# Optimization experiments

Measured on AMD Instinct MI355X. Metric: run time of the kernel, lower is better.

The kernel has to match this reference:

```python
import jax, jax.numpy as jnp
import numpy as np
import math

N_NODES = 20000
N_EDGES = 320000
DIM = 256
NUM_HEADS = 8


def setup_inputs() -> dict:
    key = jax.random.key(0)
    ks = jax.random.split(key, 8)
    x = jax.random.normal(ks[0], (N_NODES, DIM), dtype=jnp.float32)
    edge_index = jax.random.randint(ks[1], (2, N_EDGES), 0, N_NODES, dtype=jnp.int64)
    edge_attr = jax.random.normal(ks[2], (N_EDGES, DIM), dtype=jnp.float32)
    s = 1.0 / math.sqrt(DIM)
    Wq = jax.random.uniform(ks[3], (DIM, DIM), jnp.float32, -s, s)
    Wk = jax.random.uniform(ks[4], (DIM, DIM), jnp.float32, -s, s)
    Wv = jax.random.uniform(ks[5], (DIM, DIM), jnp.float32, -s, s)
    We = jax.random.uniform(ks[6], (DIM, DIM), jnp.float32, -s, s)
    be = jax.random.uniform(ks[7], (DIM,), jnp.float32, -s, s)
    return {"x": x, "edge_index": edge_index, "edge_attr": edge_attr,
            "Wq": Wq, "Wk": Wk, "Wv": Wv, "We": We, "be": be}


def reference(x, edge_index, edge_attr, Wq, Wk, Wv, We, be):
    N = x.shape[0]
    E = edge_attr.shape[0]
    H = NUM_HEADS
    C = DIM // H  # per-head channels (concat=True)
    src = edge_index[0]  # segment / attention-grouping index
    dst = edge_index[1]
    # Z = edge_attr * x[dst]  -> [E, D]
    Z = edge_attr * x[dst]
    q = x @ Wq.T          # [N, D]
    k = Z @ Wk.T          # [E, D]
    v = Z @ Wv.T          # [E, D]
    edge_out = Z @ We.T + be  # [E, D]
    # split heads
    qh = q.reshape(N, H, C)
    kh = k.reshape(E, H, C)
    vh = v.reshape(E, H, C)
    # per-edge, per-head score: sum(q[src]*k)/sqrt(C)   -> [E, H]
    scores = jnp.einsum('ehc,ehc->eh', qh[src], kh) / math.sqrt(C)
    # segment softmax grouped by src node
    m = jax.ops.segment_max(scores, src, num_segments=N)        # [N, H]
    ex = jnp.exp(scores - m[src])                               # [E, H]
    denom = jax.ops.segment_sum(ex, src, num_segments=N)        # [N, H]
    attn = ex / (denom[src] + 1e-16)                            # [E, H]
    # weighted scatter-sum of values -> [N, H, C] -> [N, D]
    out = jax.ops.segment_sum(attn[:, :, None] * vh, src, num_segments=N)
    out = out.reshape(N, H * C)
    return (out, edge_out)
```

## Files before the change

kernel.cpp:

```cpp
#include <hip/hip_runtime.h>
#include <math.h>

#define NN 20000
#define NE 320000
#define DIM 256

typedef __bf16 bf16x8 __attribute__((ext_vector_type(8)));
typedef float f32x4 __attribute__((ext_vector_type(4)));
typedef int i32x4 __attribute__((ext_vector_type(4)));
typedef unsigned short u16x4 __attribute__((ext_vector_type(4)));

union B8 { i32x4 i; bf16x8 b; };

__device__ __forceinline__ unsigned short f2bf(float f) {
  unsigned int u; __builtin_memcpy(&u, &f, 4);
  u += 0x7fffu + ((u >> 16) & 1u);
  return (unsigned short)(u >> 16);
}
__device__ __forceinline__ float bf2f(unsigned short h) {
  unsigned int u = ((unsigned int)h) << 16;
  float f; __builtin_memcpy(&f, &u, 4);
  return f;
}

#define GLOAD16(gp, lp)                                                        \
  __builtin_amdgcn_global_load_lds(                                            \
      (const __attribute__((address_space(1))) unsigned int*)(gp),             \
      (__attribute__((address_space(3))) unsigned int*)(lp), 16, 0, 0)

__global__ __launch_bounds__(256) void pack_w(const float* __restrict__ W,
                                              unsigned short* __restrict__ wf) {
  int t = blockIdx.x * 256 + threadIdx.x;
  int lane = t & 63, ct = (t >> 6) & 15, ks = t >> 10;
  int col = ct * 16 + (lane & 15);
  int k0 = ks * 32 + (lane >> 4) * 8;
  const float* src = W + col * 256 + k0;
  unsigned int h[8];
#pragma unroll
  for (int j = 0; j < 8; j++) h[j] = f2bf(src[j]);
  i32x4 v;
  v.x = (int)(h[0] | (h[1] << 16));
  v.y = (int)(h[2] | (h[3] << 16));
  v.z = (int)(h[4] | (h[5] << 16));
  v.w = (int)(h[6] | (h[7] << 16));
  ((i32x4*)wf)[t] = v;
}

__global__ __launch_bounds__(256) void zprep(const float* __restrict__ x,
                                             const int* __restrict__ ei,
                                             const float* __restrict__ ea,
                                             unsigned short* __restrict__ zg) {
  int idx = blockIdx.x * 256 + threadIdx.x;
  int e = idx >> 4, c = idx & 15;
  int dst = ei[NE + e];
  const f32x4* ap = (const f32x4*)(ea + (size_t)e * DIM + c * 16);
  const f32x4* xp = (const f32x4*)(x + (size_t)dst * DIM + c * 16);
  unsigned int h[16];
#pragma unroll
  for (int j = 0; j < 4; j++) {
    f32x4 a = ap[j], b = xp[j];
    f32x4 p = a * b;
    h[j * 4 + 0] = f2bf(p.x); h[j * 4 + 1] = f2bf(p.y);
    h[j * 4 + 2] = f2bf(p.z); h[j * 4 + 3] = f2bf(p.w);
  }
  i32x4 o0, o1;
  o0.x = (int)(h[0] | (h[1] << 16));  o0.y = (int)(h[2] | (h[3] << 16));
  o0.z = (int)(h[4] | (h[5] << 16));  o0.w = (int)(h[6] | (h[7] << 16));
  o1.x = (int)(h[8] | (h[9] << 16));  o1.y = (int)(h[10] | (h[11] << 16));
  o1.z = (int)(h[12] | (h[13] << 16)); o1.w = (int)(h[14] | (h[15] << 16));
  i32x4* dp = (i32x4*)(zg + (size_t)e * 512 + c * 16);
  dp[0] = o0; dp[1] = o1;
}

__device__ __forceinline__ void gemm_tile(const unsigned short* zs,
                                          const unsigned short* wf,
                                          int lane, int wv, f32x4 (&acc)[4][4]) {
#pragma unroll 1
  for (int ksI = 0; ksI < 8; ksI++) {
    bf16x8 afr[4], bfr[4];
#pragma unroll
    for (int rt = 0; rt < 4; rt++) {
      int row = rt * 16 + (lane & 15);
      int k = ksI * 32 + (lane >> 4) * 8;
      int byteo = (row * 512 + k * 2) ^ ((row & 7) << 4);
      B8 u; u.i = *(const i32x4*)((const char*)zs + byteo);
      afr[rt] = u.b;
    }
#pragma unroll
    for (int ct = 0; ct < 4; ct++) {
      B8 u; u.i = ((const i32x4*)wf)[ksI * 1024 + (wv * 4 + ct) * 64 + lane];
      bfr[ct] = u.b;
    }
#pragma unroll
    for (int rt = 0; rt < 4; rt++)
#pragma unroll
      for (int ct = 0; ct < 4; ct++)
        acc[rt][ct] = __builtin_amdgcn_mfma_f32_16x16x32_bf16(afr[rt], bfr[ct], acc[rt][ct], 0, 0, 0);
  }
}

__global__ __launch_bounds__(256) void q_kernel(const float* __restrict__ x,
                                                const unsigned short* __restrict__ wf,
                                                float* __restrict__ q) {
  __shared__ unsigned short zs[64 * 256];
  int tid = threadIdx.x, lane = tid & 63, wv = tid >> 6;
  int r0 = blockIdx.x * 64;
  int dcol = lane * 4;
#pragma unroll 4
  for (int rr = 0; rr < 16; rr++) {
    int r = rr * 4 + wv;
    int row = r0 + r;
    f32x4 a = {0.f, 0.f, 0.f, 0.f};
    if (row < NN) a = *(const f32x4*)(x + (size_t)row * DIM + dcol);
    u16x4 z;
    z.x = f2bf(a.x); z.y = f2bf(a.y); z.z = f2bf(a.z); z.w = f2bf(a.w);
    int byteo = (r * 512 + dcol * 2) ^ ((r & 7) << 4);
    *(u16x4*)((char*)zs + byteo) = z;
  }
  __syncthreads();
  f32x4 acc[4][4];
#pragma unroll
  for (int rt = 0; rt < 4; rt++)
#pragma unroll
    for (int ct = 0; ct < 4; ct++) acc[rt][ct] = (f32x4){0.f, 0.f, 0.f, 0.f};
  gemm_tile(zs, wf, lane, wv, acc);
  int cq = lane & 15, rq = lane >> 4;
#pragma unroll
  for (int ct = 0; ct < 4; ct++) {
    int col = wv * 64 + ct * 16 + cq;
#pragma unroll
    for (int rt = 0; rt < 4; rt++) {
#pragma unroll
      for (int j = 0; j < 4; j++) {
        int row = r0 + rt * 16 + rq * 4 + j;
        if (row < NN) q[(size_t)row * DIM + col] = acc[rt][ct][j];
      }
    }
  }
}

__global__ __launch_bounds__(512) void gemm_edge(
    const unsigned short* __restrict__ zg, const int* __restrict__ ei,
    const int* __restrict__ pos,
    const unsigned short* __restrict__ wfk, const unsigned short* __restrict__ wfv,
    const unsigned short* __restrict__ wfe, const float* __restrict__ be,
    const float* __restrict__ q, unsigned short* __restrict__ vws,
    float* __restrict__ sperm, float* __restrict__ edge_out) {
  __shared__ unsigned short zs[128 * 256];
  int tid = threadIdx.x, lane = tid & 63, wv = tid >> 6;
  int wm = wv >> 2, wn = wv & 3;
  int rq = lane >> 4, cl = lane & 15;
  int e0 = blockIdx.x * 128;

  const unsigned short* wfs[3] = {wfv, wfe, wfk};
  i32x4 wbuf[4][4];
  i32x4 zbuf[2][4];
  f32x4 acc[4][4];

#define LOADW(S, SLOT)                                                         \
  {                                                                            \
    const unsigned short* wfp = wfs[(S) >> 3];                                 \
    _Pragma("unroll") for (int a = 0; a < 4; a++)                              \
        wbuf[SLOT][a] =                                                        \
            ((const i32x4*)wfp)[((S) & 7) * 1024 + (wn * 4 + a) * 64 + lane];  \
  }
#define LOADZ(S, SLOT)                                                         \
  {                                                                            \
    _Pragma("unroll") for (int b = 0; b < 4; b++) {                            \
      int row = wm * 64 + b * 16 + cl;                                         \
      int kk = ((S) & 7) * 32 + rq * 8;                                        \
      int byteo = (row * 512 + kk * 2) ^ ((row & 7) << 4);                     \
      zbuf[SLOT][b] = *(const i32x4*)((const char*)zs + byteo);                \
    }                                                                          \
  }
#define GEMM_PASS(P)                                                           \
  _Pragma("unroll") for (int a = 0; a < 4; a++)                                \
      _Pragma("unroll") for (int b = 0; b < 4; b++)                            \
          acc[a][b] = (f32x4){0.f, 0.f, 0.f, 0.f};                             \
  _Pragma("unroll") for (int ks = 0; ks < 8; ks++) {                           \
    const int step = (P) * 8 + ks;                                             \
    if (step + 2 < 24) LOADW(step + 2, (step + 2) & 3);                        \
    if (step + 1 < 24) LOADZ(step + 1, (step + 1) & 1);                        \
    _Pragma("unroll") for (int a = 0; a < 4; a++) {                            \
      B8 w; w.i = wbuf[step & 3][a];                                           \
      _Pragma("unroll") for (int b = 0; b < 4; b++) {                          \
        B8 z; z.i = zbuf[step & 1][b];                                         \
        acc[a][b] = __builtin_amdgcn_mfma_f32_16x16x32_bf16(w.b, z.b,          \
                                                            acc[a][b], 0, 0, 0); \
      }                                                                        \
    }                                                                          \
  }

  {
    int rl = wv * 2 + (lane >> 5);
    int c = lane & 31;
#pragma unroll
    for (int s = 0; s < 8; s++) {
      int r = s * 16 + rl;
      const unsigned short* gp = zg + (size_t)(e0 + r) * 512 + ((c ^ (r & 7)) * 8);
      unsigned short* lp = zs + (s * 16 + wv * 2) * 256;
      GLOAD16(gp, lp);
    }
  }
  LOADW(0, 0); LOADW(1, 1);
  __syncthreads();
  LOADZ(0, 0); LOADZ(1, 1);

  GEMM_PASS(0)
#pragma unroll
  for (int a = 0; a < 4; a++) {
    int ch = wn * 64 + a * 16 + rq * 4;
#pragma unroll
    for (int b = 0; b < 4; b++) {
      int edge = wm * 64 + b * 16 + cl;
      u16x4 o;
      o.x = f2bf(acc[a][b][0]); o.y = f2bf(acc[a][b][1]);
      o.z = f2bf(acc[a][b][2]); o.w = f2bf(acc[a][b][3]);
      *(u16x4*)(vws + (size_t)(e0 + edge) * DIM + ch) = o;
    }
  }

  GEMM_PASS(1)
#pragma unroll
  for (int a = 0; a < 4; a++) {
    int ch = wn * 64 + a * 16 + rq * 4;
    f32x4 bias = *(const f32x4*)(be + ch);
#pragma unroll
    for (int b = 0; b < 4; b++) {
      int edge = wm * 64 + b * 16 + cl;
      f32x4 o = acc[a][b] + bias;
      *(f32x4*)(edge_out + (size_t)(e0 + edge) * DIM + ch) = o;
    }
  }

  GEMM_PASS(2)
#pragma unroll
  for (int b = 0; b < 4; b++) {
    int edge = wm * 64 + b * 16 + cl;
    int sr = ei[e0 + edge];
    int pe = pos[e0 + edge];
    const float* qp = q + (size_t)sr * DIM + wn * 64 + rq * 4;
    f32x4 q0 = *(const f32x4*)(qp);
    f32x4 q1 = *(const f32x4*)(qp + 16);
    f32x4 q2 = *(const f32x4*)(qp + 32);
    f32x4 q3 = *(const f32x4*)(qp + 48);
    float s0 = acc[0][b][0] * q0[0] + acc[0][b][1] * q0[1] +
               acc[0][b][2] * q0[2] + acc[0][b][3] * q0[3] +
               acc[1][b][0] * q1[0] + acc[1][b][1] * q1[1] +
               acc[1][b][2] * q1[2] + acc[1][b][3] * q1[3];
    float s1 = acc[2][b][0] * q2[0] + acc[2][b][1] * q2[1] +
               acc[2][b][2] * q2[2] + acc[2][b][3] * q2[3] +
               acc[3][b][0] * q3[0] + acc[3][b][1] * q3[1] +
               acc[3][b][2] * q3[2] + acc[3][b][3] * q3[3];
    s0 += __shfl_xor(s0, 16); s0 += __shfl_xor(s0, 32);
    s1 += __shfl_xor(s1, 16); s1 += __shfl_xor(s1, 32);
    if (lane < 16) {
      sperm[(size_t)pe * 8 + wn * 2 + 0] = s0 * 0.17677669529663687f;
      sperm[(size_t)pe * 8 + wn * 2 + 1] = s1 * 0.17677669529663687f;
    }
  }
#undef LOADW
#undef LOADZ
#undef GEMM_PASS
}

__global__ __launch_bounds__(256) void count_kernel(const int* __restrict__ ei,
                                                    int* __restrict__ counts) {
  int e = blockIdx.x * 256 + threadIdx.x;
  if (e < NE) atomicAdd(&counts[ei[e]], 1);
}

__global__ __launch_bounds__(256) void scan_kernel(const int* __restrict__ counts,
                                                   int* __restrict__ offs,
                                                   int* __restrict__ cursor) {
  __shared__ int tmp[256];
  __shared__ int carry;
  int tid = threadIdx.x;
  if (tid == 0) carry = 0;
  __syncthreads();
  for (int base = 0; base < NN; base += 256) {
    int i = base + tid;
    int v = (i < NN) ? counts[i] : 0;
    tmp[tid] = v;
    __syncthreads();
    for (int off = 1; off < 256; off <<= 1) {
      int t = (tid >= off) ? tmp[tid - off] : 0;
      __syncthreads();
      tmp[tid] += t;
      __syncthreads();
    }
    int incl = tmp[tid];
    int c0 = carry;
    if (i < NN) {
      offs[i] = c0 + incl - v;
      cursor[i] = c0 + incl - v;
    }
    __syncthreads();
    if (tid == 255) carry = c0 + incl;
    __syncthreads();
  }
  if (tid == 0) offs[NN] = carry;
}

__global__ __launch_bounds__(256) void fill_kernel(const int* __restrict__ ei,
                                                   int* __restrict__ cursor,
                                                   int* __restrict__ eids,
                                                   int* __restrict__ pos) {
  int e = blockIdx.x * 256 + threadIdx.x;
  if (e < NE) {
    int p = atomicAdd(&cursor[ei[e]], 1);
    eids[p] = e;
    pos[e] = p;
  }
}

__global__ __launch_bounds__(256) void node_kernel(const int* __restrict__ offs,
                                                   const int* __restrict__ eids,
                                                   const float* __restrict__ sperm,
                                                   const unsigned short* __restrict__ vws,
                                                   float* __restrict__ out) {
  int tid = threadIdx.x;
  int n = blockIdx.x * 4 + (tid >> 6);
  int lane = tid & 63, h = lane >> 3;
  int o0 = offs[n], deg = offs[n + 1] - o0;
  float m = -INFINITY, s = 0.f;
  float a0 = 0.f, a1 = 0.f, a2 = 0.f, a3 = 0.f;
  int e = (deg > 0) ? eids[o0] : 0;
  u16x4 v = *(const u16x4*)(vws + (size_t)e * DIM + lane * 4);
  for (int i = 0; i < deg; i++) {
    int en = (i + 1 < deg) ? eids[o0 + i + 1] : e;
    u16x4 vn = *(const u16x4*)(vws + (size_t)en * DIM + lane * 4);
    float sc = sperm[(size_t)(o0 + i) * 8 + h];
    float mn = fmaxf(m, sc);
    float scale = __expf(m - mn);
    float p = __expf(sc - mn);
    s = s * scale + p;
    m = mn;
    a0 = a0 * scale + p * bf2f(v.x);
    a1 = a1 * scale + p * bf2f(v.y);
    a2 = a2 * scale + p * bf2f(v.z);
    a3 = a3 * scale + p * bf2f(v.w);
    v = vn;
  }
  float inv = 1.f / (s + 1e-16f);
  f32x4 o;
  o.x = a0 * inv; o.y = a1 * inv; o.z = a2 * inv; o.w = a3 * inv;
  *(f32x4*)(out + (size_t)n * DIM + lane * 4) = o;
}

extern "C" void kernel_launch(void* const* d_in, const int* in_sizes, int n_in,
                              void* d_out, int out_size, void* d_ws, size_t ws_size,
                              hipStream_t stream) {
  const float* x = (const float*)d_in[0];
  const int* ei = (const int*)d_in[1];
  const float* ea = (const float*)d_in[2];
  const float* Wq = (const float*)d_in[3];
  const float* Wk = (const float*)d_in[4];
  const float* Wv = (const float*)d_in[5];
  const float* We = (const float*)d_in[6];
  const float* be = (const float*)d_in[7];

  float* out = (float*)d_out;
  float* edge_out = out + (size_t)NN * DIM;
  unsigned short* zg = (unsigned short*)edge_out;
  float* q = out;

  char* ws = (char*)d_ws;
  unsigned short* wfq = (unsigned short*)(ws + 0);
  unsigned short* wfk = (unsigned short*)(ws + 131072);
  unsigned short* wfv = (unsigned short*)(ws + 262144);
  unsigned short* wfe = (unsigned short*)(ws + 393216);
  unsigned short* vws = (unsigned short*)(ws + 524288);
  float* sperm = (float*)(ws + 524288 + 163840000);
  int* counts = (int*)(ws + 524288 + 163840000 + 10240000);
  int* offs   = (int*)(ws + 524288 + 163840000 + 10240000 + 80000);
  int* cursor = (int*)(ws + 524288 + 163840000 + 10240000 + 160016);
  int* eids   = (int*)(ws + 524288 + 163840000 + 10240000 + 240016);
  int* pos    = (int*)(ws + 524288 + 163840000 + 10240000 + 240016 + 1280000);

  hipMemsetAsync(counts, 0, NN * sizeof(int), stream);

  pack_w<<<32, 256, 0, stream>>>(Wq, wfq);
  pack_w<<<32, 256, 0, stream>>>(Wk, wfk);
  pack_w<<<32, 256, 0, stream>>>(Wv, wfv);
  pack_w<<<32, 256, 0, stream>>>(We, wfe);

  zprep<<<NE / 16, 256, 0, stream>>>(x, ei, ea, zg);

  count_kernel<<<(NE + 255) / 256, 256, 0, stream>>>(ei, counts);
  scan_kernel<<<1, 256, 0, stream>>>(counts, offs, cursor);
  fill_kernel<<<(NE + 255) / 256, 256, 0, stream>>>(ei, cursor, eids, pos);

  q_kernel<<<(NN + 63) / 64, 256, 0, stream>>>(x, wfq, q);

  gemm_edge<<<NE / 128, 512, 0, stream>>>(zg, ei, pos, wfk, wfv, wfe, be, q,
                                          vws, sperm, edge_out);

  node_kernel<<<NN / 4, 256, 0, stream>>>(offs, eids, sperm, vws, out);
}
```

Baseline: 619.8 us.

## Store Z in MFMA fragment order, deepen W prefetch, and use a serial-chunk scan

zprep now writes Z directly in the per-tile MFMA fragment layout, 16 bytes per thread. gemm_edge can then copy each 128-edge tile contiguously into LDS and read fragments without XOR-swizzled addressing. The weight prefetch distance grows from two steps to three. The single-block scan now has each thread serially sum a 79-element chunk and combines the chunks with wave shuffles, replacing a barrier-heavy loop over 79 iterations. The zprep grid doubles with half the work per thread. LDS reads in the new fragment layout may hit different bank patterns.

```diff
diff --git a/kernel.cpp b/kernel.cpp
--- a/kernel.cpp
+++ b/kernel.cpp
@@ -51,25 +51,27 @@
                                              const float* __restrict__ ea,
                                              unsigned short* __restrict__ zg) {
   int idx = blockIdx.x * 256 + threadIdx.x;
-  int e = idx >> 4, c = idx & 15;
+  int lane = idx & 63;
+  int bt = (idx >> 6) & 7;
+  int ks = (idx >> 9) & 7;
+  int tile = idx >> 12;
+  int e = tile * 128 + bt * 16 + (lane & 15);
+  int kf = ks * 32 + (lane >> 4) * 8;
   int dst = ei[NE + e];
-  const f32x4* ap = (const f32x4*)(ea + (size_t)e * DIM + c * 16);
-  const f32x4* xp = (const f32x4*)(x + (size_t)dst * DIM + c * 16);
-  unsigned int h[16];
-#pragma unroll
-  for (int j = 0; j < 4; j++) {
-    f32x4 a = ap[j], b = xp[j];
-    f32x4 p = a * b;
-    h[j * 4 + 0] = f2bf(p.x); h[j * 4 + 1] = f2bf(p.y);
-    h[j * 4 + 2] = f2bf(p.z); h[j * 4 + 3] = f2bf(p.w);
-  }
-  i32x4 o0, o1;
-  o0.x = (int)(h[0] | (h[1] << 16));  o0.y = (int)(h[2] | (h[3] << 16));
-  o0.z = (int)(h[4] | (h[5] << 16));  o0.w = (int)(h[6] | (h[7] << 16));
-  o1.x = (int)(h[8] | (h[9] << 16));  o1.y = (int)(h[10] | (h[11] << 16));
-  o1.z = (int)(h[12] | (h[13] << 16)); o1.w = (int)(h[14] | (h[15] << 16));
-  i32x4* dp = (i32x4*)(zg + (size_t)e * 512 + c * 16);
-  dp[0] = o0; dp[1] = o1;
+  const f32x4* ap = (const f32x4*)(ea + (size_t)e * DIM + kf);
+  const f32x4* xp = (const f32x4*)(x + (size_t)dst * DIM + kf);
+  f32x4 p0 = ap[0] * xp[0];
+  f32x4 p1 = ap[1] * xp[1];
+  unsigned int h[8];
+  h[0] = f2bf(p0.x); h[1] = f2bf(p0.y); h[2] = f2bf(p0.z); h[3] = f2bf(p0.w);
+  h[4] = f2bf(p1.x); h[5] = f2bf(p1.y); h[6] = f2bf(p1.z); h[7] = f2bf(p1.w);
+  i32x4 o;
+  o.x = (int)(h[0] | (h[1] << 16));
+  o.y = (int)(h[2] | (h[3] << 16));
+  o.z = (int)(h[4] | (h[5] << 16));
+  o.w = (int)(h[6] | (h[7] << 16));
+  size_t byteo = (size_t)tile * 131072 + (size_t)(idx & 4095) * 16;
+  *(i32x4*)((char*)zg + byteo) = o;
 }
 
 __device__ __forceinline__ void gemm_tile(const unsigned short* zs,
@@ -167,10 +169,8 @@
 #define LOADZ(S, SLOT)                                                         \
   {                                                                            \
     _Pragma("unroll") for (int b = 0; b < 4; b++) {                            \
-      int row = wm * 64 + b * 16 + cl;                                         \
-      int kk = ((S) & 7) * 32 + rq * 8;                                        \
-      int byteo = (row * 512 + kk * 2) ^ ((row & 7) << 4);                     \
-      zbuf[SLOT][b] = *(const i32x4*)((const char*)zs + byteo);                \
+      int fi = ((S) & 7) * 8 + wm * 4 + b;                                     \
+      zbuf[SLOT][b] = *(const i32x4*)(zs + fi * 512 + lane * 8);               \
     }                                                                          \
   }
 #define GEMM_PASS(P)                                                           \
@@ -179,7 +179,7 @@
           acc[a][b] = (f32x4){0.f, 0.f, 0.f, 0.f};                             \
   _Pragma("unroll") for (int ks = 0; ks < 8; ks++) {                           \
     const int step = (P) * 8 + ks;                                             \
-    if (step + 2 < 24) LOADW(step + 2, (step + 2) & 3);                        \
+    if (step + 3 < 24) LOADW(step + 3, (step + 3) & 3);                        \
     if (step + 1 < 24) LOADZ(step + 1, (step + 1) & 1);                        \
     _Pragma("unroll") for (int a = 0; a < 4; a++) {                            \
       B8 w; w.i = wbuf[step & 3][a];                                           \
@@ -192,17 +192,16 @@
   }
 
   {
-    int rl = wv * 2 + (lane >> 5);
-    int c = lane & 31;
+    const char* gbase = (const char*)zg + (size_t)blockIdx.x * 131072;
 #pragma unroll
     for (int s = 0; s < 8; s++) {
-      int r = s * 16 + rl;
-      const unsigned short* gp = zg + (size_t)(e0 + r) * 512 + ((c ^ (r & 7)) * 8);
-      unsigned short* lp = zs + (s * 16 + wv * 2) * 256;
+      int slab = wv * 8 + s;
+      const char* gp = gbase + slab * 1024 + lane * 16;
+      unsigned short* lp = zs + slab * 512;
       GLOAD16(gp, lp);
     }
   }
-  LOADW(0, 0); LOADW(1, 1);
+  LOADW(0, 0); LOADW(1, 1); LOADW(2, 2);
   __syncthreads();
   LOADZ(0, 0); LOADZ(1, 1);
 
@@ -273,33 +272,35 @@
 __global__ __launch_bounds__(256) void scan_kernel(const int* __restrict__ counts,
                                                    int* __restrict__ offs,
                                                    int* __restrict__ cursor) {
-  __shared__ int tmp[256];
-  __shared__ int carry;
+  const int CH = 79;
   int tid = threadIdx.x;
-  if (tid == 0) carry = 0;
+  int lane = tid & 63, wv = tid >> 6;
+  int b0 = tid * CH;
+  int sum = 0;
+  for (int j = 0; j < CH; j++) {
+    int i = b0 + j;
+    if (i < NN) sum += counts[i];
+  }
+  int pre = sum;
+  for (int d = 1; d < 64; d <<= 1) {
+    int t = __shfl_up(pre, d);
+    if (lane >= d) pre += t;
+  }
+  __shared__ int wsum[4];
+  if (lane == 63) wsum[wv] = pre;
   __syncthreads();
-  for (int base = 0; base < NN; base += 256) {
-    int i = base + tid;
-    int v = (i < NN) ? counts[i] : 0;
-    tmp[tid] = v;
-    __syncthreads();
-    for (int off = 1; off < 256; off <<= 1) {
-      int t = (tid >= off) ? tmp[tid - off] : 0;
-      __syncthreads();
-      tmp[tid] += t;
-      __syncthreads();
-    }
-    int incl = tmp[tid];
-    int c0 = carry;
+  int base = 0;
+  for (int w = 0; w < wv; w++) base += wsum[w];
+  int running = base + pre - sum;
+  for (int j = 0; j < CH; j++) {
+    int i = b0 + j;
     if (i < NN) {
-      offs[i] = c0 + incl - v;
-      cursor[i] = c0 + incl - v;
-    }
-    __syncthreads();
-    if (tid == 255) carry = c0 + incl;
-    __syncthreads();
-  }
-  if (tid == 0) offs[NN] = carry;
+      offs[i] = running;
+      cursor[i] = running;
+      running += counts[i];
+    }
+  }
+  if (tid == 255) offs[NN] = running;
 }
 
 __global__ __launch_bounds__(256) void fill_kernel(const int* __restrict__ ei,
@@ -385,7 +386,7 @@
   pack_w<<<32, 256, 0, stream>>>(Wv, wfv);
   pack_w<<<32, 256, 0, stream>>>(We, wfe);
 
-  zprep<<<NE / 16, 256, 0, stream>>>(x, ei, ea, zg);
+  zprep<<<NE * 32 / 256, 256, 0, stream>>>(x, ei, ea, zg);
 
   count_kernel<<<(NE + 255) / 256, 256, 0, stream>>>(ei, counts);
   scan_kernel<<<1, 256, 0, stream>>>(counts, offs, cursor);
```

After: 617.3 us. Within noise of the previous version (-0.4%).
